# Performance work log

Measured on AMD Instinct MI355X. Metric: run time of the kernel, lower is better.

Reference implementation:

```python
import jax, jax.numpy as jnp
import numpy as np
from jax import lax

EPS = 1e-5
GROUPS = 8
TDVD_RANGE = 10
SCALE = 1.0
SCALE_FACTOR = 0.5


def setup_inputs() -> dict:
    key = jax.random.key(0)
    k1, k2 = jax.random.split(key)
    x = jax.random.normal(k1, (2, 16, 64, 128, 128), dtype=jnp.float32)
    gn_weight = jnp.ones((16,), dtype=jnp.float32)
    gn_bias = jnp.zeros((16,), dtype=jnp.float32)
    threshold = jnp.ones((1,), dtype=jnp.float32)  # torch fills with 1.0
    conv_weight = jax.random.normal(k2, (16, 16, 3, 3, 3), dtype=jnp.float32) * 0.05
    return {"x": x, "gn_weight": gn_weight, "gn_bias": gn_bias,
            "threshold": threshold, "conv_weight": conv_weight}


def _group_norm(x, w, b):
    B, C, D, H, W = x.shape
    xr = x.reshape(B, GROUPS, C // GROUPS, D, H, W)
    mean = xr.mean(axis=(2, 3, 4, 5), keepdims=True)
    var = xr.var(axis=(2, 3, 4, 5), keepdims=True)
    xn = ((xr - mean) * lax.rsqrt(var + EPS)).reshape(B, C, D, H, W)
    return xn * w.reshape(1, C, 1, 1, 1) + b.reshape(1, C, 1, 1, 1)


def _tdvd_histogram(x):
    # reverseint(x * scale * scale_factor) counted into 21 bins [-10..10], as %.
    y = x * (SCALE * SCALE_FACTOR)
    v = jnp.ceil(y * (y >= 0)) + jnp.floor(y * (y <= 0))
    idx = (v + TDVD_RANGE).astype(jnp.int32)
    valid = (idx >= 0) & (idx <= 2 * TDVD_RANGE)
    hist = jnp.zeros((2 * TDVD_RANGE + 1,), jnp.float32).at[
        jnp.clip(idx, 0, 2 * TDVD_RANGE)].add(jnp.where(valid, 1.0, 0.0))
    return hist / x.size * 100.0


def _threshold_func(x, threshold):
    thr = (threshold[0] + 0.0) / SCALE  # zero_point=0, scale=1.0
    t = jnp.transpose(x, (2, 0, 1, 3, 4))  # [D,B,C,H,W]
    front, back = t[:-1], t[1:]
    d = (back - front) / thr
    d = jnp.where(jnp.abs(d) > 1.0, d, 0.0)  # Hardshrink(1.0)
    d = d * lax.stop_gradient(thr)           # .item() detaches in torch
    out = jnp.concatenate([t[:1], front + d], axis=0)
    return jnp.transpose(out, (1, 2, 0, 3, 4))


def reference(x, gn_weight, gn_bias, threshold, conv_weight):
    x = jax.nn.relu(_group_norm(x, gn_weight, gn_bias))
    hist = _tdvd_histogram(x)
    x = _threshold_func(x, threshold)
    out = lax.conv_general_dilated(
        x, conv_weight, window_strides=(1, 1, 1),
        padding=((1, 1), (1, 1), (1, 1)),
        dimension_numbers=("NCDHW", "OIDHW", "NCDHW"))
    return out, hist
```

## Files before the change

kernel.cpp:

```cpp
#include <hip/hip_runtime.h>

typedef __attribute__((ext_vector_type(8))) short short8;
typedef __attribute__((ext_vector_type(4))) float f32x4;

#define GROUP_ELEMS 2097152
#define NBLK 64

__device__ inline short f2bf(float f) {
  unsigned u = __builtin_bit_cast(unsigned, f);
  unsigned r = (u + 0x7FFFu + ((u >> 16) & 1u)) >> 16;
  return (short)r;
}

__device__ inline void gload_lds16(const void* g, void* l) {
  __builtin_amdgcn_global_load_lds(
      (const __attribute__((address_space(1))) unsigned int*)g,
      (__attribute__((address_space(3))) unsigned int*)l, 16, 0, 0);
}

__global__ __launch_bounds__(256) void k1_partials(const float* __restrict__ x,
                                                   float2* __restrict__ partials) {
  int group = blockIdx.x >> 6;
  int blk = blockIdx.x & 63;
  const float4* p = (const float4*)(x + (size_t)group * GROUP_ELEMS + (size_t)blk * 32768);
  float sum = 0.f, sq = 0.f;
  for (int i = threadIdx.x; i < 8192; i += 256) {
    float4 v = p[i];
    sum += v.x + v.y + v.z + v.w;
    sq  += v.x*v.x + v.y*v.y + v.z*v.z + v.w*v.w;
  }
  for (int off = 32; off; off >>= 1) {
    sum += __shfl_down(sum, off, 64);
    sq  += __shfl_down(sq,  off, 64);
  }
  __shared__ float2 sw[4];
  int lane = threadIdx.x & 63, wid = threadIdx.x >> 6;
  if (lane == 0) sw[wid] = make_float2(sum, sq);
  __syncthreads();
  if (threadIdx.x == 0) {
    float s = 0.f, q = 0.f;
    for (int j = 0; j < 4; ++j) { s += sw[j].x; q += sw[j].y; }
    partials[blockIdx.x] = make_float2(s, q);
  }
}

__global__ void k2_stats(const float2* __restrict__ partials,
                         float2* __restrict__ stats, int* __restrict__ hist) {
  int t = threadIdx.x;
  if (t < 16) {
    float s = 0.f, q = 0.f;
    for (int j = 0; j < NBLK; ++j) { float2 p = partials[t * NBLK + j]; s += p.x; q += p.y; }
    float mean = s / (float)GROUP_ELEMS;
    float var  = q / (float)GROUP_ELEMS - mean * mean;
    stats[t] = make_float2(mean, rsqrtf(var + 1e-5f));
  }
  if (t < 21) hist[t] = 0;
}

__global__ void k2b_wprep(const float* __restrict__ wgt, unsigned short* __restrict__ fbw2,
                          unsigned int* __restrict__ dummy) {
  int t = threadIdx.x;
  if (t < 960) {
    int f = t >> 6, lane = t & 63;
    int kd = f / 5, c = f - kd * 5;
    int m = lane & 15, g = lane >> 4;
    int icb = (g & 1) * 8, g2 = g >> 1;
    int tap = 2 * c + g2;
    short8 v;
    #pragma unroll
    for (int j = 0; j < 8; ++j)
      v[j] = (tap <= 8) ? f2bf(wgt[m * 432 + (icb + j) * 27 + kd * 9 + tap]) : (short)0;
    *(short8*)(fbw2 + t * 8) = v;
  }
  if (t >= 960 && t < 976) dummy[t - 960] = 0;
}

__global__ __launch_bounds__(256) void k3_norm_thresh_hist(
    const float* __restrict__ x, const float* __restrict__ gw, const float* __restrict__ gb,
    const float* __restrict__ thrp, const float2* __restrict__ stats,
    unsigned short* __restrict__ z, int* __restrict__ hist) {
  __shared__ int sh[21];
  int t = threadIdx.x;
  if (t < 21) sh[t] = 0;
  __syncthreads();
  int bx = blockIdx.x;
  int b = bx >> 9, part = (bx >> 2) & 127, dchunk = bx & 3;
  int cp = t >> 5, hwl = t & 31;
  int hw = part * 128 + hwl * 4;
  int c0 = cp * 2, c1 = c0 + 1;
  float2 st = stats[b * 8 + cp];
  float A0 = gw[c0] * st.y, B0 = gb[c0] - st.x * A0;
  float A1 = gw[c1] * st.y, B1 = gb[c1] - st.x * A1;
  float thr = thrp[0];
  const f32x4* px0 = (const f32x4*)(x + (size_t)(b * 16 + c0) * 1048576 + hw);
  const f32x4* px1 = (const f32x4*)(x + (size_t)(b * 16 + c1) * 1048576 + hw);
  unsigned* pz = (unsigned*)(z + ((size_t)b * 1048576 + hw) * 16 + c0);
  int c10 = 0, c11 = 0, c12 = 0;
  const int lo = dchunk * 16, dend = lo + 16;
  const int dstart = (lo == 0) ? 0 : lo - 1;
  f32x4 xv0 = px0[(size_t)dstart * 4096], xv1 = px1[(size_t)dstart * 4096];
  float yp0[4], yp1[4];
  for (int d = dstart; d < dend; ++d) {
    f32x4 n0 = {0.f,0.f,0.f,0.f}, n1 = {0.f,0.f,0.f,0.f};
    if (d + 1 < dend) { n0 = px0[(size_t)(d + 1) * 4096]; n1 = px1[(size_t)(d + 1) * 4096]; }
    bool act = (d >= lo);
    #pragma unroll
    for (int k = 0; k < 4; ++k) {
      float y0 = fmaxf(fmaf(xv0[k], A0, B0), 0.f);
      float y1 = fmaxf(fmaf(xv1[k], A1, B1), 0.f);
      if (act) {
        float v0 = ceilf(0.5f * y0);
        if (v0 == 0.f) c10++; else if (v0 == 1.f) c11++; else if (v0 == 2.f) c12++;
        else if (v0 <= 10.f) atomicAdd(&sh[(int)v0 + 10], 1);
        float v1 = ceilf(0.5f * y1);
        if (v1 == 0.f) c10++; else if (v1 == 1.f) c11++; else if (v1 == 2.f) c12++;
        else if (v1 <= 10.f) atomicAdd(&sh[(int)v1 + 10], 1);
        float z0, z1;
        if (d == 0) { z0 = y0; z1 = y1; }
        else {
          float dd0 = (y0 - yp0[k]) / thr;
          z0 = (fabsf(dd0) > 1.f) ? fmaf(dd0, thr, yp0[k]) : yp0[k];
          float dd1 = (y1 - yp1[k]) / thr;
          z1 = (fabsf(dd1) > 1.f) ? fmaf(dd1, thr, yp1[k]) : yp1[k];
        }
        unsigned u = (unsigned)(unsigned short)f2bf(z0) | ((unsigned)(unsigned short)f2bf(z1) << 16);
        pz[d * 131072 + k * 8] = u;
      }
      yp0[k] = y0; yp1[k] = y1;
    }
    xv0 = n0; xv1 = n1;
  }
  atomicAdd(&sh[10], c10);
  atomicAdd(&sh[11], c11);
  atomicAdd(&sh[12], c12);
  __syncthreads();
  if (t < 21) atomicAdd(&hist[t], sh[t]);
}

#define DT 8
#define PLANE 5440
__global__ __launch_bounds__(512, 4) void k4_conv(const unsigned short* __restrict__ z,
                                                  const unsigned short* __restrict__ fbw2,
                                                  const char* __restrict__ dummyc,
                                                  float* __restrict__ out) {
  __shared__ unsigned short lz[2 * PLANE];
  const int t = threadIdx.x;
  const int lane = t & 63, wid = t >> 6;
  const int b = blockIdx.z;
  const int d0 = blockIdx.y * DT;
  const int h0 = (blockIdx.x >> 2) * 8, w0 = (blockIdx.x & 3) * 32;
  const int m = lane & 15, g = lane >> 4;
  const int icb = (g & 1) * 8, g2 = g >> 1;

  short8 fb2[15];
  #pragma unroll
  for (int f = 0; f < 15; ++f)
    fb2[f] = *(const short8*)(fbw2 + (f * 64 + lane) * 8);

  int tco[5];
  #pragma unroll
  for (int c = 0; c < 5; ++c) {
    int tap = 2 * c + g2; if (tap > 8) tap = 8;
    tco[c] = ((tap / 3) * 34 + (tap % 3)) * 16;
  }

  const char* zbc = (const char*)(z + (size_t)b * 16777216);

  const int cbA = wid * 64;
  const int cbB = (wid == 0) ? 512 : (wid == 1) ? 576 : 616;
  const bool hasB = (wid < 3);
  long long hobA, hobB; bool hvA, hvB;
  {
    int gi, r, rem, s, ig, hg, wg;
    gi = cbA + lane; r = gi / 68; rem = gi - r * 68; s = rem >> 1; ig = rem & 1;
    hg = h0 - 1 + r; wg = w0 - 1 + s;
    hvA = ((unsigned)hg < 128u) && ((unsigned)wg < 128u);
    hobA = ((long long)(hg * 128 + wg) * 16 + ig * 8) * 2;
    gi = cbB + lane; r = gi / 68; rem = gi - r * 68; s = rem >> 1; ig = rem & 1;
    hg = h0 - 1 + r; wg = w0 - 1 + s;
    hvB = ((unsigned)hg < 128u) && ((unsigned)wg < 128u);
    hobB = ((long long)(hg * 128 + wg) * 16 + ig * 8) * 2;
  }

  const f32x4 fzero = {0.f, 0.f, 0.f, 0.f};
  f32x4 A0[2], A1[2], A2[2];
  #pragma unroll
  for (int q = 0; q < 2; ++q) { A0[q] = fzero; A1[q] = fzero; A2[q] = fzero; }

  {
    const int dg = d0 - 1;
    const long long dgo = (long long)dg * 524288;
    const bool pd = (unsigned)dg < 64u;
    gload_lds16((pd && hvA) ? zbc + dgo + hobA : dummyc, &lz[cbA * 8]);
    if (hasB)
      gload_lds16((pd && hvB) ? zbc + dgo + hobB : dummyc, &lz[cbB * 8]);
  }
  __syncthreads();

#define BODY(PH, AS, AM, AN, DOJ2, DOJ1, DOJ0, DOLOAD, DOSTORE)                         \
  {                                                                                     \
    const int ph_ = (PH);                                                               \
    if (DOLOAD) {                                                                       \
      const int dg = d0 + ph_;                                                          \
      const long long dgo = (long long)dg * 524288;                                     \
      const bool pd = (unsigned)dg < 64u;                                               \
      const unsigned sl = ((unsigned)(ph_ + 1) & 1u) * PLANE;                           \
      gload_lds16((pd && hvA) ? zbc + dgo + hobA : dummyc, &lz[sl + cbA * 8]);          \
      if (hasB)                                                                         \
        gload_lds16((pd && hvB) ? zbc + dgo + hobB : dummyc, &lz[sl + cbB * 8]);        \
    }                                                                                   \
    const unsigned su = ((unsigned)ph_ & 1u) * PLANE;                                   \
    __builtin_amdgcn_s_setprio(1);                                                      \
    _Pragma("unroll")                                                                   \
    for (int q = 0; q < 2; ++q) {                                                       \
      const int hl = wid, wt = q;                                                       \
      const int qb = (hl * 34 + wt * 16 + m) * 16 + icb + (int)su;                      \
      _Pragma("unroll")                                                                 \
      for (int c = 0; c < 5; ++c) {                                                     \
        short8 a = *(const short8*)(&lz[qb + tco[c]]);                                  \
        if (DOJ2) AN[q] = __builtin_amdgcn_mfma_f32_16x16x32_bf16(a, fb2[c], AN[q], 0, 0, 0);      \
        if (DOJ1) AM[q] = __builtin_amdgcn_mfma_f32_16x16x32_bf16(a, fb2[5 + c], AM[q], 0, 0, 0);  \
        if (DOJ0) AS[q] = __builtin_amdgcn_mfma_f32_16x16x32_bf16(a, fb2[10 + c], AS[q], 0, 0, 0); \
      }                                                                                 \
    }                                                                                   \
    __builtin_amdgcn_s_setprio(0);                                                      \
    if (DOSTORE) {                                                                      \
      const int dd = d0 + ph_ - 2;                                                      \
      _Pragma("unroll")                                                                 \
      for (int q = 0; q < 2; ++q) {                                                     \
        const int hl = wid, wt = q;                                                     \
        float* op = out + (((size_t)(b * 16 + m) * 64 + dd) * 128 + (h0 + hl)) * 128    \
                    + w0 + wt * 16 + g * 4;                                             \
        *(float4*)op = make_float4(AS[q][0], AS[q][1], AS[q][2], AS[q][3]);             \
        AS[q] = fzero;                                                                  \
      }                                                                                 \
    }                                                                                   \
    __syncthreads();                                                                    \
  }

  BODY(0, A1, A2, A0, 1, 0, 0, 1, 0)
  BODY(1, A2, A0, A1, 1, 1, 0, 1, 0)
  BODY(2, A0, A1, A2, 1, 1, 1, 1, 1)
  #pragma unroll 1
  for (int pp = 3; pp <= 6; pp += 3) {
    BODY(pp,     A1, A2, A0, 1, 1, 1, 1, 1)
    BODY(pp + 1, A2, A0, A1, 1, 1, 1, 1, 1)
    BODY(pp + 2, A0, A1, A2, 1, 1, 1, 1, 1)
  }
  BODY(9, A1, A2, A0, 0, 0, 1, 0, 1)
#undef BODY
}

__global__ void k5_hist_out(const int* __restrict__ hist, float* __restrict__ out) {
  int t = threadIdx.x;
  if (t < 21) out[33554432u + t] = (float)hist[t] * (100.0f / 33554432.0f);
}

extern "C" void kernel_launch(void* const* d_in, const int* in_sizes, int n_in,
                              void* d_out, int out_size, void* d_ws, size_t ws_size,
                              hipStream_t stream) {
  (void)in_sizes; (void)n_in; (void)out_size; (void)ws_size;
  const float* x   = (const float*)d_in[0];
  const float* gw  = (const float*)d_in[1];
  const float* gb  = (const float*)d_in[2];
  const float* thr = (const float*)d_in[3];
  const float* cw  = (const float*)d_in[4];
  float* out = (float*)d_out;

  char* ws = (char*)d_ws;
  unsigned short* z = (unsigned short*)ws;
  float2* partials  = (float2*)(ws + (size_t)67108864);
  float2* stats     = (float2*)(ws + (size_t)67108864 + 8192);
  int*    hist      = (int*)  (ws + (size_t)67108864 + 8192 + 128);
  unsigned int* dummy = (unsigned int*)(ws + (size_t)67108864 + 8448);
  unsigned short* fbw2 = (unsigned short*)(ws + (size_t)67108864 + 16384);

  k1_partials<<<1024, 256, 0, stream>>>(x, partials);
  k2_stats<<<1, 64, 0, stream>>>(partials, stats, hist);
  k2b_wprep<<<1, 1024, 0, stream>>>(cw, fbw2, dummy);
  k3_norm_thresh_hist<<<1024, 256, 0, stream>>>(x, gw, gb, thr, stats, z, hist);
  k4_conv<<<dim3(64, 8, 2), 512, 0, stream>>>(z, fbw2, (const char*)dummy, out);
  k5_hist_out<<<1, 64, 0, stream>>>(hist, out);
}
```

Baseline: 146.3 us.

## Merge small setup kernels, fold hist output into conv, remap norm kernel to columns

Merges the stats and weight-prep kernels into one launch and moves the histogram-to-output write into the first block of the conv kernel, removing two kernel launches. The norm/threshold/histogram kernel now gives each thread a single hw column that it walks across all 64 depth slices with scalar loads. Before, each thread handled 4-wide vectors over depth chunks of 16 plus one halo slice. This drops the recomputed halo slice but lengthens the serial per-thread loop and reduces bytes per load, which may lower memory-level parallelism.

After: 133.6 us. 1.09x faster.

```diff
diff --git a/kernel.cpp b/kernel.cpp
--- a/kernel.cpp
+++ b/kernel.cpp
@@ -44,8 +44,9 @@
   }
 }
 
-__global__ void k2_stats(const float2* __restrict__ partials,
-                         float2* __restrict__ stats, int* __restrict__ hist) {
+__global__ void k2_prep(const float2* __restrict__ partials, const float* __restrict__ wgt,
+                        float2* __restrict__ stats, int* __restrict__ hist,
+                        unsigned short* __restrict__ fbw2, unsigned int* __restrict__ dummy) {
   int t = threadIdx.x;
   if (t < 16) {
     float s = 0.f, q = 0.f;
@@ -55,11 +56,6 @@
     stats[t] = make_float2(mean, rsqrtf(var + 1e-5f));
   }
   if (t < 21) hist[t] = 0;
-}
-
-__global__ void k2b_wprep(const float* __restrict__ wgt, unsigned short* __restrict__ fbw2,
-                          unsigned int* __restrict__ dummy) {
-  int t = threadIdx.x;
   if (t < 960) {
     int f = t >> 6, lane = t & 63;
     int kd = f / 5, c = f - kd * 5;
@@ -83,51 +79,42 @@
   int t = threadIdx.x;
   if (t < 21) sh[t] = 0;
   __syncthreads();
-  int bx = blockIdx.x;
-  int b = bx >> 9, part = (bx >> 2) & 127, dchunk = bx & 3;
-  int cp = t >> 5, hwl = t & 31;
-  int hw = part * 128 + hwl * 4;
+  int hwl = t & 31, cp = t >> 5;
+  int b = blockIdx.x >> 9;
+  int hw = (blockIdx.x & 511) * 32 + hwl;
   int c0 = cp * 2, c1 = c0 + 1;
   float2 st = stats[b * 8 + cp];
   float A0 = gw[c0] * st.y, B0 = gb[c0] - st.x * A0;
   float A1 = gw[c1] * st.y, B1 = gb[c1] - st.x * A1;
   float thr = thrp[0];
-  const f32x4* px0 = (const f32x4*)(x + (size_t)(b * 16 + c0) * 1048576 + hw);
-  const f32x4* px1 = (const f32x4*)(x + (size_t)(b * 16 + c1) * 1048576 + hw);
-  unsigned* pz = (unsigned*)(z + ((size_t)b * 1048576 + hw) * 16 + c0);
+  const float* px0 = x + (size_t)(b * 16 + c0) * 1048576 + hw;
+  const float* px1 = x + (size_t)(b * 16 + c1) * 1048576 + hw;
+  unsigned* pz = (unsigned*)(z + ((size_t)b * 64 * 16384 + hw) * 16 + c0);
   int c10 = 0, c11 = 0, c12 = 0;
-  const int lo = dchunk * 16, dend = lo + 16;
-  const int dstart = (lo == 0) ? 0 : lo - 1;
-  f32x4 xv0 = px0[(size_t)dstart * 4096], xv1 = px1[(size_t)dstart * 4096];
-  float yp0[4], yp1[4];
-  for (int d = dstart; d < dend; ++d) {
-    f32x4 n0 = {0.f,0.f,0.f,0.f}, n1 = {0.f,0.f,0.f,0.f};
-    if (d + 1 < dend) { n0 = px0[(size_t)(d + 1) * 4096]; n1 = px1[(size_t)(d + 1) * 4096]; }
-    bool act = (d >= lo);
-    #pragma unroll
-    for (int k = 0; k < 4; ++k) {
-      float y0 = fmaxf(fmaf(xv0[k], A0, B0), 0.f);
-      float y1 = fmaxf(fmaf(xv1[k], A1, B1), 0.f);
-      if (act) {
-        float v0 = ceilf(0.5f * y0);
-        if (v0 == 0.f) c10++; else if (v0 == 1.f) c11++; else if (v0 == 2.f) c12++;
-        else if (v0 <= 10.f) atomicAdd(&sh[(int)v0 + 10], 1);
-        float v1 = ceilf(0.5f * y1);
-        if (v1 == 0.f) c10++; else if (v1 == 1.f) c11++; else if (v1 == 2.f) c12++;
-        else if (v1 <= 10.f) atomicAdd(&sh[(int)v1 + 10], 1);
-        float z0, z1;
-        if (d == 0) { z0 = y0; z1 = y1; }
-        else {
-          float dd0 = (y0 - yp0[k]) / thr;
-          z0 = (fabsf(dd0) > 1.f) ? fmaf(dd0, thr, yp0[k]) : yp0[k];
-          float dd1 = (y1 - yp1[k]) / thr;
-          z1 = (fabsf(dd1) > 1.f) ? fmaf(dd1, thr, yp1[k]) : yp1[k];
-        }
-        unsigned u = (unsigned)(unsigned short)f2bf(z0) | ((unsigned)(unsigned short)f2bf(z1) << 16);
-        pz[d * 131072 + k * 8] = u;
-      }
-      yp0[k] = y0; yp1[k] = y1;
+  float xv0 = px0[0], xv1 = px1[0];
+  float yp0 = 0.f, yp1 = 0.f;
+  for (int d = 0; d < 64; ++d) {
+    float n0 = 0.f, n1 = 0.f;
+    if (d < 63) { n0 = px0[(d + 1) * 16384]; n1 = px1[(d + 1) * 16384]; }
+    float y0 = fmaxf(fmaf(xv0, A0, B0), 0.f);
+    float y1 = fmaxf(fmaf(xv1, A1, B1), 0.f);
+    float v0 = ceilf(0.5f * y0);
+    if (v0 == 0.f) c10++; else if (v0 == 1.f) c11++; else if (v0 == 2.f) c12++;
+    else if (v0 <= 10.f) atomicAdd(&sh[(int)v0 + 10], 1);
+    float v1 = ceilf(0.5f * y1);
+    if (v1 == 0.f) c10++; else if (v1 == 1.f) c11++; else if (v1 == 2.f) c12++;
+    else if (v1 <= 10.f) atomicAdd(&sh[(int)v1 + 10], 1);
+    float z0, z1;
+    if (d == 0) { z0 = y0; z1 = y1; }
+    else {
+      float dd0 = (y0 - yp0) / thr;
+      z0 = (fabsf(dd0) > 1.f) ? fmaf(dd0, thr, yp0) : yp0;
+      float dd1 = (y1 - yp1) / thr;
+      z1 = (fabsf(dd1) > 1.f) ? fmaf(dd1, thr, yp1) : yp1;
     }
+    unsigned u = (unsigned)(unsigned short)f2bf(z0) | ((unsigned)(unsigned short)f2bf(z1) << 16);
+    pz[d * 131072] = u;
+    yp0 = y0; yp1 = y1;
     xv0 = n0; xv1 = n1;
   }
   atomicAdd(&sh[10], c10);
@@ -142,9 +129,12 @@
 __global__ __launch_bounds__(512, 4) void k4_conv(const unsigned short* __restrict__ z,
                                                   const unsigned short* __restrict__ fbw2,
                                                   const char* __restrict__ dummyc,
+                                                  const int* __restrict__ hist,
                                                   float* __restrict__ out) {
   __shared__ unsigned short lz[2 * PLANE];
   const int t = threadIdx.x;
+  if (blockIdx.x == 0 && blockIdx.y == 0 && blockIdx.z == 0 && t < 21)
+    out[33554432u + t] = (float)hist[t] * (100.0f / 33554432.0f);
   const int lane = t & 63, wid = t >> 6;
   const int b = blockIdx.z;
   const int d0 = blockIdx.y * DT;
@@ -251,11 +241,6 @@
 #undef BODY
 }
 
-__global__ void k5_hist_out(const int* __restrict__ hist, float* __restrict__ out) {
-  int t = threadIdx.x;
-  if (t < 21) out[33554432u + t] = (float)hist[t] * (100.0f / 33554432.0f);
-}
-
 extern "C" void kernel_launch(void* const* d_in, const int* in_sizes, int n_in,
                               void* d_out, int out_size, void* d_ws, size_t ws_size,
                               hipStream_t stream) {
@@ -276,9 +261,7 @@
   unsigned short* fbw2 = (unsigned short*)(ws + (size_t)67108864 + 16384);
 
   k1_partials<<<1024, 256, 0, stream>>>(x, partials);
-  k2_stats<<<1, 64, 0, stream>>>(partials, stats, hist);
-  k2b_wprep<<<1, 1024, 0, stream>>>(cw, fbw2, dummy);
+  k2_prep<<<1, 1024, 0, stream>>>(partials, cw, stats, hist, fbw2, dummy);
   k3_norm_thresh_hist<<<1024, 256, 0, stream>>>(x, gw, gb, thr, stats, z, hist);
-  k4_conv<<<dim3(64, 8, 2), 512, 0, stream>>>(z, fbw2, (const char*)dummy, out);
-  k5_hist_out<<<1, 64, 0, stream>>>(hist, out);
-}
+  k4_conv<<<dim3(64, 8, 2), 512, 0, stream>>>(z, fbw2, (const char*)dummy, hist, out);
+}
```
